# Performance work log

Measured on AMD Instinct MI355X. Metric: run time of the kernel, lower is better.

## Reference

```python
import jax, jax.numpy as jnp
import numpy as np

L, P = 16384, 512
DT_MIN, DT_MAX = 0.001, 0.1
THRESHOLD = 1.0  # spike threshold assumed for cartesian_spike


def setup_inputs() -> dict:
    key = jax.random.key(0)
    k1, k2, k3, k4, k5, k6 = jax.random.split(key, 6)
    u = jax.random.normal(k1, (L, P), dtype=jnp.float32)
    # Stored Lambda param: [..., 0] = log(-Re(Lambda)) with Re(Lambda) < 0, [..., 1] = Im(Lambda)
    lam_real_neg = jax.random.uniform(k2, (P,), minval=0.1, maxval=1.0)  # -Re(Lambda)
    lam_imag = jax.random.normal(k3, (P,)) * 3.0
    Lambda = jnp.stack([jnp.log(lam_real_neg), lam_imag], axis=-1).astype(jnp.float32)
    # init_log_steps: log(dt) uniform in [log(dt_min), log(dt_max)], shape (P, 1)
    log_step = (np.log(DT_MIN) + jax.random.uniform(k4, (P, 1)) * (np.log(DT_MAX) - np.log(DT_MIN))).astype(jnp.float32)
    V_re = jax.random.normal(k5, (P, P), dtype=jnp.float32) / np.sqrt(P)
    V_im = jax.random.normal(k6, (P, P), dtype=jnp.float32) / np.sqrt(P)
    return {"u": u, "Lambda": Lambda, "log_step": log_step, "V_re": V_re, "V_im": V_im}


def _binop(q_i, q_j):
    A_i, b_i = q_i
    A_j, b_j = q_j
    return (A_j * A_i, A_j * b_i + b_j)


def reference(u, Lambda, log_step, V_re, V_im):
    # keep_imag = False: u stays real. discretization = 'zoh', activation = 'cartesian_spike'.
    Lambda_tilde = -jnp.exp(Lambda[..., 0]) + 1j * Lambda[..., 1]            # (P,) complex
    step = jnp.exp(log_step[:, 0])                                            # (P,)
    Lambda_bar = jnp.exp(Lambda_tilde * step)                                 # (P,) |.|<1
    # B_tilde = I, so zoh gives B_bar = diag((Lambda_bar - 1)/Lambda); B_bar @ u_t = coef * u_t
    B_coef = (Lambda_bar - 1.0) / Lambda_tilde                                # (P,)
    Lambda_elements = jnp.broadcast_to(Lambda_bar, (u.shape[0], Lambda_bar.shape[0]))
    Bu_elements = B_coef[None, :] * u.astype(Lambda_bar.dtype)                # (L, P) complex
    _, xs = jax.lax.associative_scan(_binop, (Lambda_elements, Bu_elements))  # (L, P)
    V = V_re + 1j * V_im
    xs = xs @ V.T                                                             # vmap(V @ x) over L
    spikes = (xs.real > THRESHOLD).astype(jnp.float32)                        # cartesian_spike
    return spikes
```

## Files before the change

kernel.cpp:

```cpp
#include <hip/hip_runtime.h>

#define L_LEN   16384
#define P_DIM   512
#define CHUNK   64
#define NCHUNK  256

#define KDIM    1024
#define NDIM    512
#define BM      128
#define BN      128
#define BK      64

typedef __bf16 bf16_t;
typedef __bf16 bf16x8 __attribute__((ext_vector_type(8)));
typedef float  floatx4 __attribute__((ext_vector_type(4)));

__device__ __forceinline__ void channel_consts(const float* __restrict__ Lam,
                                               const float* __restrict__ lstep,
                                               int p, float& ar, float& ai,
                                               float& br, float& bi) {
    float lr = -expf(Lam[2 * p + 0]);
    float li = Lam[2 * p + 1];
    float s  = expf(lstep[p]);
    float er = expf(lr * s);
    ar = er * cosf(li * s);
    ai = er * sinf(li * s);
    float dr = ar - 1.0f, di = ai;
    float inv = 1.0f / (lr * lr + li * li);
    br = (dr * lr + di * li) * inv;
    bi = (di * lr - dr * li) * inv;
}

__global__ void __launch_bounds__(P_DIM) k_scan_ends(const float* __restrict__ u,
        const float* __restrict__ Lam, const float* __restrict__ lstep,
        float2* __restrict__ endv) {
    int p = threadIdx.x;
    int c = blockIdx.x;
    float ar, ai, br, bi;
    channel_consts(Lam, lstep, p, ar, ai, br, bi);
    float xr = 0.f, xi = 0.f;
    const float* up = u + (size_t)c * CHUNK * P_DIM + p;
    #pragma unroll 8
    for (int k = 0; k < CHUNK; ++k) {
        float uv = up[(size_t)k * P_DIM];
        float nr = ar * xr - ai * xi + br * uv;
        float ni = ar * xi + ai * xr + bi * uv;
        xr = nr; xi = ni;
    }
    endv[(size_t)c * P_DIM + p] = make_float2(xr, xi);
}

__global__ void __launch_bounds__(1024) k_carry(const float* __restrict__ Lam,
        const float* __restrict__ lstep, const float2* __restrict__ endv,
        float2* __restrict__ carry) {
    __shared__ float2 zl[4 * (NCHUNK + 2)];
    int tid = threadIdx.x;
    int g = tid & 3;
    int c = tid >> 2;
    int p = blockIdx.x * 4 + g;
    int zi_base = g * (NCHUNK + 2);

    float lr = -expf(Lam[2 * p + 0]);
    float li = Lam[2 * p + 1];
    float s  = expf(lstep[p]);
    float t  = s * (float)CHUNK;
    float er = expf(lr * t);
    float Ar = er * cosf(li * t);
    float Ai = er * sinf(li * t);

    float2 e = endv[(size_t)c * P_DIM + p];
    float zr = e.x, zi = e.y;
    zl[zi_base + c] = make_float2(zr, zi);
    __syncthreads();
    for (int st = 1; st < NCHUNK; st <<= 1) {
        float tr = 0.f, ti = 0.f;
        if (c >= st) { float2 v = zl[zi_base + c - st]; tr = v.x; ti = v.y; }
        __syncthreads();
        zr += Ar * tr - Ai * ti;
        zi += Ar * ti + Ai * tr;
        zl[zi_base + c] = make_float2(zr, zi);
        float nAr = Ar * Ar - Ai * Ai;
        float nAi = 2.f * Ar * Ai;
        Ar = nAr; Ai = nAi;
        __syncthreads();
    }
    float2 cv = make_float2(0.f, 0.f);
    if (c > 0) cv = zl[zi_base + c - 1];
    carry[(size_t)c * P_DIM + p] = cv;
}

__global__ void __launch_bounds__(P_DIM) k_materialize(const float* __restrict__ u,
        const float* __restrict__ Lam, const float* __restrict__ lstep,
        const float2* __restrict__ carry, bf16_t* __restrict__ A) {
    int p = threadIdx.x;
    int c = blockIdx.x;
    float ar, ai, br, bi;
    channel_consts(Lam, lstep, p, ar, ai, br, bi);
    float2 x0 = carry[(size_t)c * P_DIM + p];
    float xr = x0.x, xi = x0.y;
    const float* up = u + (size_t)c * CHUNK * P_DIM + p;
    uint32_t* Ap = (uint32_t*)(A + (size_t)c * CHUNK * KDIM) + p;
    #pragma unroll 4
    for (int k = 0; k < CHUNK; ++k) {
        float uv = up[(size_t)k * P_DIM];
        float nr = ar * xr - ai * xi + br * uv;
        float ni = ar * xi + ai * xr + bi * uv;
        xr = nr; xi = ni;
        bf16_t hr = (bf16_t)xr, hi = (bf16_t)xi;
        uint32_t pk = (uint32_t)__builtin_bit_cast(unsigned short, hr)
                    | ((uint32_t)__builtin_bit_cast(unsigned short, hi) << 16);
        Ap[(size_t)k * (KDIM / 2)] = pk;
    }
}

__global__ void __launch_bounds__(256) k_bt(const float* __restrict__ Vre,
        const float* __restrict__ Vim, bf16_t* __restrict__ Bt) {
    int idx = blockIdx.x * 256 + threadIdx.x;
    bf16_t r = (bf16_t)Vre[idx];
    bf16_t m = (bf16_t)(-Vim[idx]);
    uint32_t pk = (uint32_t)__builtin_bit_cast(unsigned short, r)
                | ((uint32_t)__builtin_bit_cast(unsigned short, m) << 16);
    ((uint32_t*)Bt)[idx] = pk;
}

__global__ void __launch_bounds__(256) k_gemm(const bf16_t* __restrict__ A,
        const bf16_t* __restrict__ Bt, float* __restrict__ out) {
    __shared__ uint4 As4[BM * BK * 2 / 16];
    __shared__ uint4 Bs4[BN * BK * 2 / 16];

    const int tid  = threadIdx.x;
    const int lane = tid & 63;
    const int w    = tid >> 6;
    const int m0   = blockIdx.x * BM;
    const int n0   = blockIdx.y * BN;
    const int wm   = (w >> 1) * 64;
    const int wn   = (w & 1) * 64;

    const int fr_m = lane & 15;
    const int fr_g = lane >> 4;

    floatx4 acc[4][4];
    #pragma unroll
    for (int i = 0; i < 4; ++i)
        #pragma unroll
        for (int j = 0; j < 4; ++j) {
            floatx4 z = {0.f, 0.f, 0.f, 0.f};
            acc[i][j] = z;
        }

    const bf16_t* Asrc = A  + (size_t)m0 * KDIM;
    const bf16_t* Bsrc = Bt + (size_t)n0 * KDIM;

    const bf16_t* ga[4]; const bf16_t* gb[4];
    char* la[4]; char* lb[4];
    #pragma unroll
    for (int i = 0; i < 4; ++i) {
        int q   = i * 256 + tid;
        int row = q >> 3;
        int gc  = (q & 7) ^ (row & 7);
        ga[i] = Asrc + (size_t)row * KDIM + gc * 8;
        gb[i] = Bsrc + (size_t)row * KDIM + gc * 8;
        la[i] = (char*)As4 + (size_t)q * 16;
        lb[i] = (char*)Bs4 + (size_t)q * 16;
    }

    for (int kt = 0; kt < KDIM; kt += BK) {
        __syncthreads();
        #pragma unroll
        for (int i = 0; i < 4; ++i) {
            __builtin_amdgcn_global_load_lds(
                (const __attribute__((address_space(1))) void*)(ga[i] + kt),
                (__attribute__((address_space(3))) void*)la[i], 16, 0, 0);
            __builtin_amdgcn_global_load_lds(
                (const __attribute__((address_space(1))) void*)(gb[i] + kt),
                (__attribute__((address_space(3))) void*)lb[i], 16, 0, 0);
        }
        __syncthreads();
        #pragma unroll
        for (int kk = 0; kk < BK; kk += 32) {
            bf16x8 af[4], bf[4];
            #pragma unroll
            for (int i = 0; i < 4; ++i) {
                int m  = wm + i * 16 + fr_m;
                int cc = (kk >> 3) + fr_g;
                int sc = cc ^ (m & 7);
                af[i] = *(const bf16x8*)((const bf16_t*)As4 + m * BK + sc * 8);
            }
            #pragma unroll
            for (int j = 0; j < 4; ++j) {
                int n  = wn + j * 16 + fr_m;
                int cc = (kk >> 3) + fr_g;
                int sc = cc ^ (n & 7);
                bf[j] = *(const bf16x8*)((const bf16_t*)Bs4 + n * BK + sc * 8);
            }
            #pragma unroll
            for (int i = 0; i < 4; ++i)
                #pragma unroll
                for (int j = 0; j < 4; ++j)
                    acc[i][j] = __builtin_amdgcn_mfma_f32_16x16x32_bf16(
                        af[i], bf[j], acc[i][j], 0, 0, 0);
        }
    }

    #pragma unroll
    for (int i = 0; i < 4; ++i)
        #pragma unroll
        for (int j = 0; j < 4; ++j)
            #pragma unroll
            for (int r = 0; r < 4; ++r) {
                int rr = wm + i * 16 + fr_g * 4 + r;
                int cl = wn + j * 16 + fr_m;
                float v = acc[i][j][r];
                out[(size_t)(m0 + rr) * NDIM + (n0 + cl)] = (v > 1.0f) ? 1.0f : 0.0f;
            }
}

extern "C" void kernel_launch(void* const* d_in, const int* in_sizes, int n_in,
                              void* d_out, int out_size, void* d_ws, size_t ws_size,
                              hipStream_t stream) {
    (void)in_sizes; (void)n_in; (void)out_size; (void)ws_size;
    const float* u     = (const float*)d_in[0];
    const float* Lam   = (const float*)d_in[1];
    const float* lstep = (const float*)d_in[2];
    const float* Vre   = (const float*)d_in[3];
    const float* Vim   = (const float*)d_in[4];
    float* out = (float*)d_out;

    char* ws = (char*)d_ws;
    const size_t endv_bytes  = (size_t)NCHUNK * P_DIM * sizeof(float2);
    const size_t carry_bytes = endv_bytes;
    const size_t bt_bytes    = (size_t)NDIM * KDIM * sizeof(bf16_t);
    float2* endv  = (float2*)(ws);
    float2* carry = (float2*)(ws + endv_bytes);
    bf16_t* Bt    = (bf16_t*)(ws + endv_bytes + carry_bytes);
    bf16_t* A     = (bf16_t*)(ws + endv_bytes + carry_bytes + bt_bytes);

    hipLaunchKernelGGL(k_scan_ends, dim3(NCHUNK), dim3(P_DIM), 0, stream,
                       u, Lam, lstep, endv);
    hipLaunchKernelGGL(k_bt, dim3(NDIM * P_DIM / 256), dim3(256), 0, stream,
                       Vre, Vim, Bt);
    hipLaunchKernelGGL(k_carry, dim3(P_DIM / 4), dim3(1024), 0, stream,
                       Lam, lstep, endv, carry);
    hipLaunchKernelGGL(k_materialize, dim3(NCHUNK), dim3(P_DIM), 0, stream,
                       u, Lam, lstep, carry, A);
    hipLaunchKernelGGL(k_gemm, dim3(L_LEN / BM, NDIM / BN), dim3(256), 0, stream,
                       A, Bt, out);
}
```

Baseline: 128.4 us.

## Halve scan chunk, fuse V conversion into scan, vectorise channels, shrink GEMM tile

Halves the chunk length so the scan kernels launch twice as many blocks, and has each thread process two channels with float2 loads and uint2 packed stores. The Vre/Vim-to-bf16 conversion is folded into the chunk-end scan kernel, removing one launch. The GEMM N tile drops from 128 to 64 with a launch-bounds occupancy hint, giving more workgroups to spread over the CUs. The trade-off is a longer carry scan (512 chunks, 2 channels per block) and less data reuse per GEMM tile.

```diff
diff --git a/kernel.cpp b/kernel.cpp
--- a/kernel.cpp
+++ b/kernel.cpp
@@ -2,26 +2,31 @@
 
 #define L_LEN   16384
 #define P_DIM   512
-#define CHUNK   64
-#define NCHUNK  256
+#define CHUNK   32
+#define NCHUNK  512
 
 #define KDIM    1024
 #define NDIM    512
 #define BM      128
-#define BN      128
+#define BN      64
 #define BK      64
 
 typedef __bf16 bf16_t;
 typedef __bf16 bf16x8 __attribute__((ext_vector_type(8)));
 typedef float  floatx4 __attribute__((ext_vector_type(4)));
 
-__device__ __forceinline__ void channel_consts(const float* __restrict__ Lam,
-                                               const float* __restrict__ lstep,
-                                               int p, float& ar, float& ai,
-                                               float& br, float& bi) {
-    float lr = -expf(Lam[2 * p + 0]);
-    float li = Lam[2 * p + 1];
-    float s  = expf(lstep[p]);
+__device__ __forceinline__ uint32_t pack_bf16(float a, float b) {
+    bf16_t ha = (bf16_t)a, hb = (bf16_t)b;
+    return (uint32_t)__builtin_bit_cast(unsigned short, ha)
+         | ((uint32_t)__builtin_bit_cast(unsigned short, hb) << 16);
+}
+
+__device__ __forceinline__ void ch_consts(float lam0, float lam1, float ls,
+                                          float& ar, float& ai,
+                                          float& br, float& bi) {
+    float lr = -expf(lam0);
+    float li = lam1;
+    float s  = expf(ls);
     float er = expf(lr * s);
     ar = er * cosf(li * s);
     ai = er * sinf(li * s);
@@ -31,99 +36,109 @@
     bi = (di * lr - dr * li) * inv;
 }
 
-__global__ void __launch_bounds__(P_DIM) k_scan_ends(const float* __restrict__ u,
+__global__ void __launch_bounds__(256) k_scan_ends(const float* __restrict__ u,
         const float* __restrict__ Lam, const float* __restrict__ lstep,
-        float2* __restrict__ endv) {
-    int p = threadIdx.x;
-    int c = blockIdx.x;
-    float ar, ai, br, bi;
-    channel_consts(Lam, lstep, p, ar, ai, br, bi);
-    float xr = 0.f, xi = 0.f;
-    const float* up = u + (size_t)c * CHUNK * P_DIM + p;
+        const float* __restrict__ Vre, const float* __restrict__ Vim,
+        float2* __restrict__ endv, bf16_t* __restrict__ Bt) {
+    const int t = threadIdx.x;
+    const int c = blockIdx.x;
+
+    {
+        int idx = c * 256 + t;
+        float2 vr = ((const float2*)Vre)[idx];
+        float2 vi = ((const float2*)Vim)[idx];
+        ((uint2*)Bt)[idx] = make_uint2(pack_bf16(vr.x, -vi.x),
+                                       pack_bf16(vr.y, -vi.y));
+    }
+
+    float4 lam4 = ((const float4*)Lam)[t];
+    float2 ls2  = ((const float2*)lstep)[t];
+    float ar0, ai0, br0, bi0, ar1, ai1, br1, bi1;
+    ch_consts(lam4.x, lam4.y, ls2.x, ar0, ai0, br0, bi0);
+    ch_consts(lam4.z, lam4.w, ls2.y, ar1, ai1, br1, bi1);
+
+    float xr0 = 0.f, xi0 = 0.f, xr1 = 0.f, xi1 = 0.f;
+    const float2* up = (const float2*)(u + (size_t)c * CHUNK * P_DIM) + t;
     #pragma unroll 8
     for (int k = 0; k < CHUNK; ++k) {
-        float uv = up[(size_t)k * P_DIM];
-        float nr = ar * xr - ai * xi + br * uv;
-        float ni = ar * xi + ai * xr + bi * uv;
-        xr = nr; xi = ni;
-    }
-    endv[(size_t)c * P_DIM + p] = make_float2(xr, xi);
+        float2 uv = up[(size_t)k * (P_DIM / 2)];
+        float nr0 = ar0 * xr0 - ai0 * xi0 + br0 * uv.x;
+        float ni0 = ar0 * xi0 + ai0 * xr0 + bi0 * uv.x;
+        float nr1 = ar1 * xr1 - ai1 * xi1 + br1 * uv.y;
+        float ni1 = ar1 * xi1 + ai1 * xr1 + bi1 * uv.y;
+        xr0 = nr0; xi0 = ni0; xr1 = nr1; xi1 = ni1;
+    }
+    ((float4*)endv)[c * 256 + t] = make_float4(xr0, xi0, xr1, xi1);
 }
 
 __global__ void __launch_bounds__(1024) k_carry(const float* __restrict__ Lam,
         const float* __restrict__ lstep, const float2* __restrict__ endv,
         float2* __restrict__ carry) {
-    __shared__ float2 zl[4 * (NCHUNK + 2)];
-    int tid = threadIdx.x;
-    int g = tid & 3;
-    int c = tid >> 2;
-    int p = blockIdx.x * 4 + g;
-    int zi_base = g * (NCHUNK + 2);
+    __shared__ float2 zl[NCHUNK * 2];
+    const int tid = threadIdx.x;
+    const int g = tid & 1;
+    const int c = tid >> 1;
+    const int p = blockIdx.x * 2 + g;
 
     float lr = -expf(Lam[2 * p + 0]);
     float li = Lam[2 * p + 1];
     float s  = expf(lstep[p]);
-    float t  = s * (float)CHUNK;
-    float er = expf(lr * t);
-    float Ar = er * cosf(li * t);
-    float Ai = er * sinf(li * t);
+    float tt = s * (float)CHUNK;
+    float er = expf(lr * tt);
+    float Ar = er * cosf(li * tt);
+    float Ai = er * sinf(li * tt);
 
     float2 e = endv[(size_t)c * P_DIM + p];
     float zr = e.x, zi = e.y;
-    zl[zi_base + c] = make_float2(zr, zi);
+    zl[c * 2 + g] = make_float2(zr, zi);
     __syncthreads();
     for (int st = 1; st < NCHUNK; st <<= 1) {
         float tr = 0.f, ti = 0.f;
-        if (c >= st) { float2 v = zl[zi_base + c - st]; tr = v.x; ti = v.y; }
+        if (c >= st) { float2 v = zl[(c - st) * 2 + g]; tr = v.x; ti = v.y; }
         __syncthreads();
         zr += Ar * tr - Ai * ti;
         zi += Ar * ti + Ai * tr;
-        zl[zi_base + c] = make_float2(zr, zi);
+        zl[c * 2 + g] = make_float2(zr, zi);
         float nAr = Ar * Ar - Ai * Ai;
         float nAi = 2.f * Ar * Ai;
         Ar = nAr; Ai = nAi;
         __syncthreads();
     }
     float2 cv = make_float2(0.f, 0.f);
-    if (c > 0) cv = zl[zi_base + c - 1];
+    if (c > 0) cv = zl[(c - 1) * 2 + g];
     carry[(size_t)c * P_DIM + p] = cv;
 }
 
-__global__ void __launch_bounds__(P_DIM) k_materialize(const float* __restrict__ u,
+__global__ void __launch_bounds__(256) k_materialize(const float* __restrict__ u,
         const float* __restrict__ Lam, const float* __restrict__ lstep,
         const float2* __restrict__ carry, bf16_t* __restrict__ A) {
-    int p = threadIdx.x;
-    int c = blockIdx.x;
-    float ar, ai, br, bi;
-    channel_consts(Lam, lstep, p, ar, ai, br, bi);
-    float2 x0 = carry[(size_t)c * P_DIM + p];
-    float xr = x0.x, xi = x0.y;
-    const float* up = u + (size_t)c * CHUNK * P_DIM + p;
-    uint32_t* Ap = (uint32_t*)(A + (size_t)c * CHUNK * KDIM) + p;
+    const int t = threadIdx.x;
+    const int c = blockIdx.x;
+
+    float4 lam4 = ((const float4*)Lam)[t];
+    float2 ls2  = ((const float2*)lstep)[t];
+    float ar0, ai0, br0, bi0, ar1, ai1, br1, bi1;
+    ch_consts(lam4.x, lam4.y, ls2.x, ar0, ai0, br0, bi0);
+    ch_consts(lam4.z, lam4.w, ls2.y, ar1, ai1, br1, bi1);
+
+    float4 cv = ((const float4*)carry)[c * 256 + t];
+    float xr0 = cv.x, xi0 = cv.y, xr1 = cv.z, xi1 = cv.w;
+    const float2* up = (const float2*)(u + (size_t)c * CHUNK * P_DIM) + t;
+    uint2* Ap = (uint2*)(A + (size_t)c * CHUNK * KDIM) + t;
     #pragma unroll 4
     for (int k = 0; k < CHUNK; ++k) {
-        float uv = up[(size_t)k * P_DIM];
-        float nr = ar * xr - ai * xi + br * uv;
-        float ni = ar * xi + ai * xr + bi * uv;
-        xr = nr; xi = ni;
-        bf16_t hr = (bf16_t)xr, hi = (bf16_t)xi;
-        uint32_t pk = (uint32_t)__builtin_bit_cast(unsigned short, hr)
-                    | ((uint32_t)__builtin_bit_cast(unsigned short, hi) << 16);
-        Ap[(size_t)k * (KDIM / 2)] = pk;
-    }
-}
-
-__global__ void __launch_bounds__(256) k_bt(const float* __restrict__ Vre,
-        const float* __restrict__ Vim, bf16_t* __restrict__ Bt) {
-    int idx = blockIdx.x * 256 + threadIdx.x;
-    bf16_t r = (bf16_t)Vre[idx];
-    bf16_t m = (bf16_t)(-Vim[idx]);
-    uint32_t pk = (uint32_t)__builtin_bit_cast(unsigned short, r)
-                | ((uint32_t)__builtin_bit_cast(unsigned short, m) << 16);
-    ((uint32_t*)Bt)[idx] = pk;
-}
-
-__global__ void __launch_bounds__(256) k_gemm(const bf16_t* __restrict__ A,
+        float2 uv = up[(size_t)k * (P_DIM / 2)];
+        float nr0 = ar0 * xr0 - ai0 * xi0 + br0 * uv.x;
+        float ni0 = ar0 * xi0 + ai0 * xr0 + bi0 * uv.x;
+        float nr1 = ar1 * xr1 - ai1 * xi1 + br1 * uv.y;
+        float ni1 = ar1 * xi1 + ai1 * xr1 + bi1 * uv.y;
+        xr0 = nr0; xi0 = ni0; xr1 = nr1; xi1 = ni1;
+        Ap[(size_t)k * 256] = make_uint2(pack_bf16(xr0, xi0),
+                                         pack_bf16(xr1, xi1));
+    }
+}
+
+__global__ void __launch_bounds__(256, 4) k_gemm(const bf16_t* __restrict__ A,
         const bf16_t* __restrict__ Bt, float* __restrict__ out) {
     __shared__ uint4 As4[BM * BK * 2 / 16];
     __shared__ uint4 Bs4[BN * BK * 2 / 16];
@@ -134,16 +149,16 @@
     const int m0   = blockIdx.x * BM;
     const int n0   = blockIdx.y * BN;
     const int wm   = (w >> 1) * 64;
-    const int wn   = (w & 1) * 64;
+    const int wn   = (w & 1) * 32;
 
     const int fr_m = lane & 15;
     const int fr_g = lane >> 4;
 
-    floatx4 acc[4][4];
+    floatx4 acc[4][2];
     #pragma unroll
     for (int i = 0; i < 4; ++i)
         #pragma unroll
-        for (int j = 0; j < 4; ++j) {
+        for (int j = 0; j < 2; ++j) {
             floatx4 z = {0.f, 0.f, 0.f, 0.f};
             acc[i][j] = z;
         }
@@ -151,34 +166,41 @@
     const bf16_t* Asrc = A  + (size_t)m0 * KDIM;
     const bf16_t* Bsrc = Bt + (size_t)n0 * KDIM;
 
-    const bf16_t* ga[4]; const bf16_t* gb[4];
-    char* la[4]; char* lb[4];
+    const bf16_t* ga[4]; char* la[4];
+    const bf16_t* gb[2]; char* lb[2];
     #pragma unroll
     for (int i = 0; i < 4; ++i) {
         int q   = i * 256 + tid;
         int row = q >> 3;
         int gc  = (q & 7) ^ (row & 7);
         ga[i] = Asrc + (size_t)row * KDIM + gc * 8;
+        la[i] = (char*)As4 + (size_t)q * 16;
+    }
+    #pragma unroll
+    for (int i = 0; i < 2; ++i) {
+        int q   = i * 256 + tid;
+        int row = q >> 3;
+        int gc  = (q & 7) ^ (row & 7);
         gb[i] = Bsrc + (size_t)row * KDIM + gc * 8;
-        la[i] = (char*)As4 + (size_t)q * 16;
         lb[i] = (char*)Bs4 + (size_t)q * 16;
     }
 
     for (int kt = 0; kt < KDIM; kt += BK) {
         __syncthreads();
         #pragma unroll
-        for (int i = 0; i < 4; ++i) {
+        for (int i = 0; i < 4; ++i)
             __builtin_amdgcn_global_load_lds(
                 (const __attribute__((address_space(1))) void*)(ga[i] + kt),
                 (__attribute__((address_space(3))) void*)la[i], 16, 0, 0);
+        #pragma unroll
+        for (int i = 0; i < 2; ++i)
             __builtin_amdgcn_global_load_lds(
                 (const __attribute__((address_space(1))) void*)(gb[i] + kt),
                 (__attribute__((address_space(3))) void*)lb[i], 16, 0, 0);
-        }
         __syncthreads();
         #pragma unroll
         for (int kk = 0; kk < BK; kk += 32) {
-            bf16x8 af[4], bf[4];
+            bf16x8 af[4], bf[2];
             #pragma unroll
             for (int i = 0; i < 4; ++i) {
                 int m  = wm + i * 16 + fr_m;
@@ -187,7 +209,7 @@
                 af[i] = *(const bf16x8*)((const bf16_t*)As4 + m * BK + sc * 8);
             }
             #pragma unroll
-            for (int j = 0; j < 4; ++j) {
+            for (int j = 0; j < 2; ++j) {
                 int n  = wn + j * 16 + fr_m;
                 int cc = (kk >> 3) + fr_g;
                 int sc = cc ^ (n & 7);
@@ -196,7 +218,7 @@
             #pragma unroll
             for (int i = 0; i < 4; ++i)
                 #pragma unroll
-                for (int j = 0; j < 4; ++j)
+                for (int j = 0; j < 2; ++j)
                     acc[i][j] = __builtin_amdgcn_mfma_f32_16x16x32_bf16(
                         af[i], bf[j], acc[i][j], 0, 0, 0);
         }
@@ -205,7 +227,7 @@
     #pragma unroll
     for (int i = 0; i < 4; ++i)
         #pragma unroll
-        for (int j = 0; j < 4; ++j)
+        for (int j = 0; j < 2; ++j)
             #pragma unroll
             for (int r = 0; r < 4; ++r) {
                 int rr = wm + i * 16 + fr_g * 4 + r;
@@ -235,13 +257,11 @@
     bf16_t* Bt    = (bf16_t*)(ws + endv_bytes + carry_bytes);
     bf16_t* A     = (bf16_t*)(ws + endv_bytes + carry_bytes + bt_bytes);
 
-    hipLaunchKernelGGL(k_scan_ends, dim3(NCHUNK), dim3(P_DIM), 0, stream,
-                       u, Lam, lstep, endv);
-    hipLaunchKernelGGL(k_bt, dim3(NDIM * P_DIM / 256), dim3(256), 0, stream,
-                       Vre, Vim, Bt);
-    hipLaunchKernelGGL(k_carry, dim3(P_DIM / 4), dim3(1024), 0, stream,
+    hipLaunchKernelGGL(k_scan_ends, dim3(NCHUNK), dim3(256), 0, stream,
+                       u, Lam, lstep, Vre, Vim, endv, Bt);
+    hipLaunchKernelGGL(k_carry, dim3(P_DIM / 2), dim3(1024), 0, stream,
                        Lam, lstep, endv, carry);
-    hipLaunchKernelGGL(k_materialize, dim3(NCHUNK), dim3(P_DIM), 0, stream,
+    hipLaunchKernelGGL(k_materialize, dim3(NCHUNK), dim3(256), 0, stream,
                        u, Lam, lstep, carry, A);
     hipLaunchKernelGGL(k_gemm, dim3(L_LEN / BM, NDIM / BN), dim3(256), 0, stream,
                        A, Bt, out);
```

After: 127.8 us (median of 2 runs). About the same (-0.5%).
